# Kernel tuning notes

Measured on AMD Instinct MI355X. Metric: run time of the kernel, lower is better.

## Reference

```python
import jax, jax.numpy as jnp
import numpy as np

TAU = 0.2
ALPHA = 0.8
LAM_POS = 1.5  # extrapolation lambda (hard positives)
EPS = 1e-8


def _cosine_sim(e):
    # torch F.cosine_similarity with eps=1e-8 norm clamping
    n = jnp.maximum(jnp.linalg.norm(e, axis=1), EPS)
    return (e @ e.T) / (n[:, None] * n[None, :])


def setup_inputs() -> dict:
    key = jax.random.key(0)
    N, D = 4096, 128
    emb = jax.random.normal(key, (N, D), dtype=jnp.float32)
    k = jnp.arange(N // 2, dtype=jnp.int32)
    i, j = 2 * k, 2 * k + 1
    # disjoint positive pairs, both orientations (matches symmetric set semantics)
    pp = jnp.concatenate([jnp.stack([i, j], 1), jnp.stack([j, i], 1)], 0)
    return {"embeddings": emb, "positive_pairs": pp, "stage_train": 1}


def reference(embeddings, positive_pairs, stage_train):
    N = embeddings.shape[0]
    pi, pj = positive_pairs[:, 0], positive_pairs[:, 1]
    Mp = jnp.zeros((N, N), dtype=bool).at[pi, pj].set(True)  # symmetric (both dirs in pairs)
    eye = jnp.eye(N, dtype=bool)
    Mn = (~eye) & (~Mp)  # negative pair mask

    # hard positive extrapolation: 1.5*e_i - 0.5*e_j (pairs disjoint -> order-free)
    hard_pos = jnp.zeros_like(embeddings).at[pi].set(
        LAM_POS * embeddings[pi] + (1.0 - LAM_POS) * embeddings[pj])

    # hard negative interpolation: loop over negatives in row-major order, last write
    idx = jnp.arange(N, dtype=jnp.int32)
    posmat = idx[:, None] * N + idx[None, :]          # enumeration position of pair (i,j)
    A = jnp.where(Mn, posmat, -1)
    col_max, col_arg = A.max(axis=0), A.argmax(axis=0)  # m as second element of (i,m)
    row_max, row_arg = A.max(axis=1), A.argmax(axis=1)  # m as first element of (m,j)
    partner = jnp.where(col_max > row_max, col_arg, row_arg)
    hard_neg = 0.5 * (embeddings + embeddings[partner])

    sim = _cosine_sim(embeddings)
    sim = jnp.where(Mp, _cosine_sim(hard_pos), jnp.where(Mn, _cosine_sim(hard_neg), sim))

    # contrastive loss with quantile hard mining
    mask = eye | Mp
    exp_sim = jnp.exp(sim / TAU)
    exp_masked = jnp.where(mask, 0.0, exp_sim)
    pos_ij = exp_sim[pi, pj]
    pos_ji = exp_sim[pj, pi]
    ei = exp_masked[pi]  # [2P, N]
    ej = exp_masked[pj]
    if stage_train:
        ti = jnp.quantile(ei, ALPHA, axis=1, keepdims=True)
        tj = jnp.quantile(ej, ALPHA, axis=1, keepdims=True)
        si = jnp.where(ei >= ti, ei, 0.0).sum(axis=1)
        sj = jnp.where(ej >= tj, ej, 0.0).sum(axis=1)
    else:
        si = ei.sum(axis=1)
        sj = ej.sum(axis=1)
    loss_ij = -jnp.log(pos_ij / (pos_ij + si))
    loss_ji = -jnp.log(pos_ji / (pos_ji + sj))
    num_pairs = positive_pairs.shape[0]
    return (loss_ij + loss_ji).sum() / (2 * num_pairs)
```

## Files before the change

### kernel.cpp

```cpp
#include <hip/hip_runtime.h>
#include <hip/hip_bf16.h>
#include <math.h>

#define D 128
#define INV_TAU 5.0f

typedef short bf16x8 __attribute__((ext_vector_type(8)));
typedef unsigned short u16x8 __attribute__((ext_vector_type(8)));
typedef float f32x4 __attribute__((ext_vector_type(4)));

__device__ __forceinline__ unsigned short bf16_bits(float v) {
    __hip_bfloat16 hb = __float2bfloat16(v);
    return *(unsigned short*)&hb;
}

__global__ void scatter_pos(const int* __restrict__ pp, int* __restrict__ pos,
                            float* __restrict__ out, int K) {
    int k = blockIdx.x * blockDim.x + threadIdx.x;
    if (k == 0) *out = 0.0f;
    if (k < K) pos[pp[2 * k]] = pp[2 * k + 1];
}

__global__ void prep_kernel(const float* __restrict__ emb, const int* __restrict__ pos,
                            const int* __restrict__ pp, unsigned short* __restrict__ hnn,
                            float* __restrict__ hpn, int N) {
    int b = blockIdx.x, d = threadIdx.x;
    __shared__ int sP;
    __shared__ float tmp[2];
    bool isHn = (b < N);
    if (isHn && d == 0) {
        int r = b, posr = pos[r];
        int jmax = -1;
        for (int j = N - 1; j >= 0; --j)
            if (j != r && j != posr) { jmax = j; break; }
        int imax = -1;
        for (int i = N - 1; i >= 0; --i)
            if (i != r && pos[i] != r) { imax = i; break; }
        long long rowm = (jmax >= 0) ? (long long)r * N + jmax : -1;
        long long colm = (imax >= 0) ? (long long)imax * N + r : -1;
        sP = (colm > rowm) ? (imax < 0 ? 0 : imax) : (jmax < 0 ? 0 : jmax);
    }
    __syncthreads();
    float h;
    int outrow;
    if (isHn) {
        int p = sP;
        h = 0.5f * (emb[b * D + d] + emb[p * D + d]);
        outrow = b;
    } else {
        int k = b - N;
        int a = pp[2 * k], bb = pp[2 * k + 1];
        h = 1.5f * emb[a * D + d] - 0.5f * emb[bb * D + d];
        outrow = a;
    }
    float ss = h * h;
#pragma unroll
    for (int off = 32; off > 0; off >>= 1) ss += __shfl_down(ss, off);
    if ((d & 63) == 0) tmp[d >> 6] = ss;
    __syncthreads();
    float inv = 1.0f / fmaxf(sqrtf(tmp[0] + tmp[1]), 1e-8f);
    if (isHn)
        hnn[outrow * D + d] = bf16_bits(h * inv);
    else
        hpn[outrow * D + d] = h * inv;
}

__global__ __launch_bounds__(256) void gemm_sim(const unsigned short* __restrict__ hnn,
                                                const int* __restrict__ pos,
                                                unsigned short* __restrict__ sims, int N) {
    __shared__ unsigned short As[128 * 136];
    __shared__ unsigned short Bs[128 * 136];
    __shared__ int pos_s[128];
    int tid = threadIdx.x;
    int rowBase = blockIdx.y * 128, colBase = blockIdx.x * 128;
    if (tid < 128) pos_s[tid] = pos[rowBase + tid];

    u16x8 ra[8], rb[8];
#pragma unroll
    for (int i = 0; i < 8; ++i) {
        int idx = i * 256 + tid;
        int row = idx >> 4, seg = idx & 15;
        ra[i] = *(const u16x8*)&hnn[(size_t)(rowBase + row) * D + seg * 8];
        rb[i] = *(const u16x8*)&hnn[(size_t)(colBase + row) * D + seg * 8];
    }
#pragma unroll
    for (int i = 0; i < 8; ++i) {
        int idx = i * 256 + tid;
        int row = idx >> 4, seg = idx & 15;
        *(u16x8*)&As[row * 136 + seg * 8] = ra[i];
        *(u16x8*)&Bs[row * 136 + seg * 8] = rb[i];
    }
    __syncthreads();

    int wave = tid >> 6, lane = tid & 63;
    int quad = lane >> 4, l15 = lane & 15;
    int rowhalf = wave >> 1, colhalf = wave & 1;

    f32x4 acc[4][4] = {};
#pragma unroll
    for (int kk = 0; kk < 4; ++kk) {
        bf16x8 af[4], bf[4];
#pragma unroll
        for (int rt = 0; rt < 4; ++rt)
            af[rt] = *(const bf16x8*)&As[(rowhalf * 64 + rt * 16 + l15) * 136 + kk * 32 + quad * 8];
#pragma unroll
        for (int ct = 0; ct < 4; ++ct)
            bf[ct] = *(const bf16x8*)&Bs[(colhalf * 64 + ct * 16 + l15) * 136 + kk * 32 + quad * 8];
#pragma unroll
        for (int rt = 0; rt < 4; ++rt)
#pragma unroll
            for (int ct = 0; ct < 4; ++ct)
                acc[rt][ct] = __builtin_amdgcn_mfma_f32_16x16x32_bf16(af[rt], bf[ct],
                                                                     acc[rt][ct], 0, 0, 0);
    }
    __syncthreads();

#pragma unroll
    for (int rt = 0; rt < 4; ++rt) {
#pragma unroll
        for (int rg = 0; rg < 4; ++rg) {
            int rloc = rowhalf * 64 + rt * 16 + quad * 4 + rg;
            int r = rowBase + rloc;
            int pr = pos_s[rloc];
#pragma unroll
            for (int ct = 0; ct < 4; ++ct) {
                int cloc = colhalf * 64 + ct * 16 + l15;
                int c = colBase + cloc;
                unsigned short u = bf16_bits(acc[rt][ct][rg]);
                unsigned short sv = (u & 0x8000u) ? (unsigned short)~u
                                                  : (unsigned short)(u | 0x8000u);
                if (c == r || c == pr) sv = 0x0080;
                As[rloc * 136 + cloc] = sv;
            }
        }
    }
    __syncthreads();

#pragma unroll
    for (int i = 0; i < 8; ++i) {
        int idx = i * 256 + tid;
        int row = idx >> 4, seg = idx & 15;
        *(u16x8*)&sims[(size_t)(rowBase + row) * N + colBase + seg * 8] =
            *(const u16x8*)&As[row * 136 + seg * 8];
    }
}

__global__ __launch_bounds__(512) void select_loss_kernel(
    const unsigned short* __restrict__ sims, const int* __restrict__ stage,
    const float* __restrict__ hpn, const int* __restrict__ pos,
    float* __restrict__ s_out, float* __restrict__ out, int N, int K, int q) {
    int wave = threadIdx.x >> 6, lane = threadIdx.x & 63;
    int row = blockIdx.x * 8 + wave;
    const unsigned short* rp = sims + (size_t)row * N;

    unsigned s[64];
#pragma unroll
    for (int j = 0; j < 8; ++j) {
        u16x8 t = *(const u16x8*)&rp[j * 512 + lane * 8];
#pragma unroll
        for (int e = 0; e < 8; ++e) s[j * 8 + e] = (unsigned)(unsigned short)t[e];
    }

    unsigned T = 0;
    if (stage[0]) {
#pragma unroll
        for (int b = 15; b >= 0; --b) {
            unsigned cand = T | (1u << b);
            int cnt = 0;
#pragma unroll
            for (int i = 0; i < 64; ++i)
                cnt += (int)__popcll(__ballot(s[i] < cand));
            if (cnt <= q) T = cand;
        }
    }

    float sum = 0.0f;
#pragma unroll
    for (int i = 0; i < 64; ++i) {
        if (s[i] >= T) {
            unsigned raw = (s[i] & 0x8000u) ? (s[i] ^ 0x8000u) : (~s[i] & 0xFFFFu);
            sum += __expf(__uint_as_float(raw << 16) * INV_TAU);
        }
    }
#pragma unroll
    for (int off = 1; off < 64; off <<= 1) sum += __shfl_xor(sum, off);
    if (lane == 0) s_out[row] = sum;

    int pr = pos[row];
    float dsum = hpn[(size_t)row * D + lane] * hpn[(size_t)pr * D + lane] +
                 hpn[(size_t)row * D + lane + 64] * hpn[(size_t)pr * D + lane + 64];
#pragma unroll
    for (int off = 32; off > 0; off >>= 1) dsum += __shfl_down(dsum, off);
    __shared__ float red[8];
    if (lane == 0) {
        float p = __expf(dsum * INV_TAU);
        red[wave] = log1pf(sum / p);
    }
    __syncthreads();
    if (threadIdx.x == 0) {
        float tot = 0.0f;
#pragma unroll
        for (int w = 0; w < 8; ++w) tot += red[w];
        atomicAdd(out, tot / (float)K);
    }
}

extern "C" void kernel_launch(void* const* d_in, const int* in_sizes, int n_in,
                              void* d_out, int out_size, void* d_ws, size_t ws_size,
                              hipStream_t stream) {
    const float* emb = (const float*)d_in[0];
    const int* pp = (const int*)d_in[1];
    const int* stage = (const int*)d_in[2];
    int N = in_sizes[0] / D;
    int K = in_sizes[1] / 2;

    char* ws = (char*)d_ws;
    size_t offPos = 0;
    size_t offHnn = offPos + (size_t)N * 4;
    size_t offHpn = offHnn + (size_t)N * D * 2;
    size_t offS = offHpn + (size_t)N * D * 4;
    size_t offSims = offS + (size_t)N * 4;
    int* pos = (int*)(ws + offPos);
    unsigned short* hnn = (unsigned short*)(ws + offHnn);
    float* hpn = (float*)(ws + offHpn);
    float* s = (float*)(ws + offS);
    unsigned short* sims = (unsigned short*)(ws + offSims);

    scatter_pos<<<(K + 255) / 256, 256, 0, stream>>>(pp, pos, (float*)d_out, K);
    prep_kernel<<<N + K, D, 0, stream>>>(emb, pos, pp, hnn, hpn, N);
    dim3 g(N / 128, N / 128);
    gemm_sim<<<g, 256, 0, stream>>>(hnn, pos, sims, N);
    int q = (int)(0.8 * (double)(N - 1));
    select_loss_kernel<<<N / 8, 512, 0, stream>>>(sims, stage, hpn, pos, s,
                                                  (float*)d_out, N, K, q);
}
```

Before: 115.3 us.

## Fuse pair scatter and hard-sample prep into one per-pair kernel

Merges the positive-index scatter and the hard negative/positive normalization into a single kernel launched once per positive pair. The serial per-row search for the last negative partner is replaced by a closed form: the largest index that is neither the row nor its positive. It also drops the unused per-row sum output. This relies on every row appearing exactly once as the first element of a pair (disjoint, symmetric pairs covering all rows), which the input construction provides.

```diff
diff --git a/kernel.cpp b/kernel.cpp
--- a/kernel.cpp
+++ b/kernel.cpp
@@ -14,55 +14,35 @@
     return *(unsigned short*)&hb;
 }
 
-__global__ void scatter_pos(const int* __restrict__ pp, int* __restrict__ pos,
-                            float* __restrict__ out, int K) {
-    int k = blockIdx.x * blockDim.x + threadIdx.x;
-    if (k == 0) *out = 0.0f;
-    if (k < K) pos[pp[2 * k]] = pp[2 * k + 1];
-}
-
-__global__ void prep_kernel(const float* __restrict__ emb, const int* __restrict__ pos,
-                            const int* __restrict__ pp, unsigned short* __restrict__ hnn,
-                            float* __restrict__ hpn, int N) {
-    int b = blockIdx.x, d = threadIdx.x;
-    __shared__ int sP;
-    __shared__ float tmp[2];
-    bool isHn = (b < N);
-    if (isHn && d == 0) {
-        int r = b, posr = pos[r];
-        int jmax = -1;
-        for (int j = N - 1; j >= 0; --j)
-            if (j != r && j != posr) { jmax = j; break; }
-        int imax = -1;
-        for (int i = N - 1; i >= 0; --i)
-            if (i != r && pos[i] != r) { imax = i; break; }
-        long long rowm = (jmax >= 0) ? (long long)r * N + jmax : -1;
-        long long colm = (imax >= 0) ? (long long)imax * N + r : -1;
-        sP = (colm > rowm) ? (imax < 0 ? 0 : imax) : (jmax < 0 ? 0 : jmax);
-    }
-    __syncthreads();
-    float h;
-    int outrow;
-    if (isHn) {
-        int p = sP;
-        h = 0.5f * (emb[b * D + d] + emb[p * D + d]);
-        outrow = b;
-    } else {
-        int k = b - N;
-        int a = pp[2 * k], bb = pp[2 * k + 1];
-        h = 1.5f * emb[a * D + d] - 0.5f * emb[bb * D + d];
-        outrow = a;
-    }
-    float ss = h * h;
-#pragma unroll
-    for (int off = 32; off > 0; off >>= 1) ss += __shfl_down(ss, off);
-    if ((d & 63) == 0) tmp[d >> 6] = ss;
-    __syncthreads();
-    float inv = 1.0f / fmaxf(sqrtf(tmp[0] + tmp[1]), 1e-8f);
-    if (isHn)
-        hnn[outrow * D + d] = bf16_bits(h * inv);
-    else
-        hpn[outrow * D + d] = h * inv;
+__global__ void prep_pair_kernel(const float* __restrict__ emb, const int* __restrict__ pp,
+                                 int* __restrict__ pos, unsigned short* __restrict__ hnn,
+                                 float* __restrict__ hpn, float* __restrict__ out,
+                                 int N, int K) {
+    int k = blockIdx.x, d = threadIdx.x;
+    int a = pp[2 * k], b = pp[2 * k + 1];
+    if (k == 0 && d == 0) *out = 0.0f;
+    if (d == 0) pos[a] = b;
+    int p = N - 1;
+    if (p == a || p == b) p = N - 2;
+    if (p == a || p == b) p = N - 3;
+
+    float ea = emb[(size_t)a * D + d];
+    float hn = 0.5f * (ea + emb[(size_t)p * D + d]);
+    float hp = 1.5f * ea - 0.5f * emb[(size_t)b * D + d];
+
+    float sn = hn * hn, sp = hp * hp;
+#pragma unroll
+    for (int off = 32; off > 0; off >>= 1) {
+        sn += __shfl_down(sn, off);
+        sp += __shfl_down(sp, off);
+    }
+    __shared__ float tn[2], tp[2];
+    if ((d & 63) == 0) { tn[d >> 6] = sn; tp[d >> 6] = sp; }
+    __syncthreads();
+    float invn = 1.0f / fmaxf(sqrtf(tn[0] + tn[1]), 1e-8f);
+    float invp = 1.0f / fmaxf(sqrtf(tp[0] + tp[1]), 1e-8f);
+    hnn[(size_t)a * D + d] = bf16_bits(hn * invn);
+    hpn[(size_t)a * D + d] = hp * invp;
 }
 
 __global__ __launch_bounds__(256) void gemm_sim(const unsigned short* __restrict__ hnn,
@@ -148,7 +128,7 @@
 __global__ __launch_bounds__(512) void select_loss_kernel(
     const unsigned short* __restrict__ sims, const int* __restrict__ stage,
     const float* __restrict__ hpn, const int* __restrict__ pos,
-    float* __restrict__ s_out, float* __restrict__ out, int N, int K, int q) {
+    float* __restrict__ out, int N, int K, int q) {
     int wave = threadIdx.x >> 6, lane = threadIdx.x & 63;
     int row = blockIdx.x * 8 + wave;
     const unsigned short* rp = sims + (size_t)row * N;
@@ -184,7 +164,6 @@
     }
 #pragma unroll
     for (int off = 1; off < 64; off <<= 1) sum += __shfl_xor(sum, off);
-    if (lane == 0) s_out[row] = sum;
 
     int pr = pos[row];
     float dsum = hpn[(size_t)row * D + lane] * hpn[(size_t)pr * D + lane] +
@@ -218,19 +197,16 @@
     size_t offPos = 0;
     size_t offHnn = offPos + (size_t)N * 4;
     size_t offHpn = offHnn + (size_t)N * D * 2;
-    size_t offS = offHpn + (size_t)N * D * 4;
-    size_t offSims = offS + (size_t)N * 4;
+    size_t offSims = offHpn + (size_t)N * D * 4;
     int* pos = (int*)(ws + offPos);
     unsigned short* hnn = (unsigned short*)(ws + offHnn);
     float* hpn = (float*)(ws + offHpn);
-    float* s = (float*)(ws + offS);
     unsigned short* sims = (unsigned short*)(ws + offSims);
 
-    scatter_pos<<<(K + 255) / 256, 256, 0, stream>>>(pp, pos, (float*)d_out, K);
-    prep_kernel<<<N + K, D, 0, stream>>>(emb, pos, pp, hnn, hpn, N);
+    prep_pair_kernel<<<K, D, 0, stream>>>(emb, pp, pos, hnn, hpn, (float*)d_out, N, K);
     dim3 g(N / 128, N / 128);
     gemm_sim<<<g, 256, 0, stream>>>(hnn, pos, sims, N);
     int q = (int)(0.8 * (double)(N - 1));
-    select_loss_kernel<<<N / 8, 512, 0, stream>>>(sims, stage, hpn, pos, s,
+    select_loss_kernel<<<N / 8, 512, 0, stream>>>(sims, stage, hpn, pos,
                                                   (float*)d_out, N, K, q);
 }
```

Measured after the change: 111.9 us. -2.9%, faster.
